# Performance work log

Hardware: AMD Instinct MI355X
Metric: run time of the kernel (lower is better)

## Reference

```python
import jax, jax.numpy as jnp
import numpy as np

DIM = 1024
NUM_HEADS = 16
NUM_KV_HEADS = 4
HEAD_DIM = DIM // NUM_HEADS  # 64
GROUP = NUM_HEADS // NUM_KV_HEADS  # 4
SCALE = HEAD_DIM ** -0.5


def setup_inputs() -> dict:
    key = jax.random.key(0)
    ks = jax.random.split(key, 6)
    B, N = 2, 2048
    x = jax.random.normal(ks[0], (B, N, DIM), dtype=jnp.float32)
    s = DIM ** -0.5
    Wq = jax.random.normal(ks[1], (DIM, DIM), dtype=jnp.float32) * s
    Wk = jax.random.normal(ks[2], (DIM, NUM_KV_HEADS * HEAD_DIM), dtype=jnp.float32) * s
    Wv = jax.random.normal(ks[3], (DIM, NUM_KV_HEADS * HEAD_DIM), dtype=jnp.float32) * s
    Wo = jax.random.normal(ks[4], (DIM, DIM), dtype=jnp.float32) * s
    bo = jax.random.normal(ks[5], (DIM,), dtype=jnp.float32) * 0.01
    return {"x": x, "Wq": Wq, "Wk": Wk, "Wv": Wv, "Wo": Wo, "bo": bo}


def reference(x, Wq, Wk, Wv, Wo, bo):
    B, N, C = x.shape
    # projections
    q = (x @ Wq).reshape(B, N, NUM_HEADS, HEAD_DIM)          # B N H D
    k = (x @ Wk).reshape(B, N, NUM_KV_HEADS, HEAD_DIM)       # B N Kh D
    v = (x @ Wv).reshape(B, N, NUM_KV_HEADS, HEAD_DIM)
    # group query heads: H = Kh * GROUP; broadcast KV per group (no repeat copy)
    q = q.reshape(B, N, NUM_KV_HEADS, GROUP, HEAD_DIM)
    # scores: B Kh G Nq Nk
    attn = jnp.einsum('bqhgd,bkhd->bhgqk', q, k) * SCALE
    attn = jax.nn.softmax(attn, axis=-1)
    out = jnp.einsum('bhgqk,bkhd->bqhgd', attn, v)           # B N Kh G D
    out = out.reshape(B, N, C)
    return out @ Wo + bo
```

## Files before the change

kernel.cpp:

```cpp
#include <hip/hip_runtime.h>


typedef unsigned short u16;
typedef short s8 __attribute__((ext_vector_type(8)));
typedef float f4 __attribute__((ext_vector_type(4)));
typedef u16 u16x4 __attribute__((ext_vector_type(4)));

__device__ __forceinline__ u16 f2bf(float f) {
  unsigned u = __float_as_uint(f);
  u += 0x7fff + ((u >> 16) & 1);
  return (u16)(u >> 16);
}

__device__ __forceinline__ void glds16(const u16* g, u16* l) {
  __builtin_amdgcn_global_load_lds((const __attribute__((address_space(1))) unsigned*)g,
                                   (__attribute__((address_space(3))) unsigned*)l, 16, 0, 0);
}

__global__ __launch_bounds__(256) void cvt_x(const float* __restrict__ x, u16* __restrict__ xb) {
  const int n4 = (4096 * 1024) / 4;
  for (int i = blockIdx.x * 256 + threadIdx.x; i < n4; i += gridDim.x * 256) {
    float4 f = ((const float4*)x)[i];
    u16x4 o = { f2bf(f.x), f2bf(f.y), f2bf(f.z), f2bf(f.w) };
    ((u16x4*)xb)[i] = o;
  }
}

__global__ __launch_bounds__(256) void cvt_w(const float* __restrict__ Wq, const float* __restrict__ Wk,
                                             const float* __restrict__ Wv, const float* __restrict__ Wo,
                                             u16* __restrict__ wqkvt, u16* __restrict__ wot) {
  const int N1 = 1536 * 1024, NT = N1 + 1024 * 1024;
  for (int i = blockIdx.x * 256 + threadIdx.x; i < NT; i += gridDim.x * 256) {
    if (i < N1) {
      int n = i >> 10, k = i & 1023;
      float v;
      if (n < 1024)      v = Wq[(k << 10) + n] * 0.125f;
      else if (n < 1280) v = Wk[(k << 8) + (n - 1024)];
      else               v = Wv[(k << 8) + (n - 1280)];
      wqkvt[i] = f2bf(v);
    } else {
      int j = i - N1;
      int n = j >> 10, k = j & 1023;
      wot[j] = f2bf(Wo[(k << 10) + n]);
    }
  }
}

template<int MODE>
__global__ __launch_bounds__(256) void gemm_bt(const u16* __restrict__ A, const u16* __restrict__ Bt,
                                               u16* __restrict__ Cq, u16* __restrict__ Vt,
                                               float* __restrict__ Cf, const float* __restrict__ bias,
                                               const int K) {
  __shared__ u16 As[128 * 32];
  __shared__ u16 Bs[128 * 32];
  const int tid = threadIdx.x, lane = tid & 63, w = tid >> 6;
  const int wm = w >> 1, wn = w & 1;
  const int m0 = blockIdx.y * 128, n0 = blockIdx.x * 128;
  const int g = lane >> 4, c = lane & 15;
  const int srow = w * 32 + (lane >> 2), scol = (lane & 3) * 8;
  const u16* ga = A + (m0 + srow) * K + scol;
  const u16* gb = Bt + (n0 + srow) * K + scol;
  f4 acc[4][4] = {};
  for (int k0 = 0; k0 < K; k0 += 32) {
    glds16(ga,           &As[w * 1024]);
    glds16(ga + 16 * K,  &As[w * 1024 + 512]);
    glds16(gb,           &Bs[w * 1024]);
    glds16(gb + 16 * K,  &Bs[w * 1024 + 512]);
    ga += 32; gb += 32;
    __syncthreads();
    s8 a[4], b[4];
#pragma unroll
    for (int m = 0; m < 4; ++m) a[m] = *(const s8*)&As[(wm * 64 + m * 16 + c) * 32 + g * 8];
#pragma unroll
    for (int n = 0; n < 4; ++n) b[n] = *(const s8*)&Bs[(wn * 64 + n * 16 + c) * 32 + g * 8];
#pragma unroll
    for (int m = 0; m < 4; ++m)
#pragma unroll
      for (int n = 0; n < 4; ++n)
        acc[m][n] = __builtin_amdgcn_mfma_f32_16x16x32_bf16(a[m], b[n], acc[m][n], 0, 0, 0);
    __syncthreads();
  }
#pragma unroll
  for (int m = 0; m < 4; ++m) {
#pragma unroll
    for (int n = 0; n < 4; ++n) {
#pragma unroll
      for (int r = 0; r < 4; ++r) {
        const int row = m0 + wm * 64 + m * 16 + g * 4 + r;
        const int col = n0 + wn * 64 + n * 16 + c;
        if (MODE == 0) {
          const u16 hv = f2bf(acc[m][n][r]);
          if (col < 1280) {
            Cq[row * 1536 + col] = hv;
          } else {
            const int cc = col - 1280, kh = cc >> 6, dd = cc & 63;
            const int bb = row >> 11, tok = row & 2047;
            Vt[(((bb << 2) + kh) * 64 + dd) * 2048 + tok] = hv;
          }
        } else {
          Cf[row * 1024 + col] = acc[m][n][r] + bias[col];
        }
      }
    }
  }
}

__global__ __launch_bounds__(256) void attn_fwd(const u16* __restrict__ qkv, const u16* __restrict__ vt,
                                                u16* __restrict__ ao) {
  __shared__ u16 QP[64 * 64];
  __shared__ u16 Ks[64 * 64];
  __shared__ u16 Vs[64 * 64];
  const int tid = threadIdx.x, lane = tid & 63, w = tid >> 6;
  const int h = blockIdx.y, b = blockIdx.z, kh = h >> 2;
  const int q0 = blockIdx.x * 64;
  const int g = lane >> 4, c = lane & 15;
  const int srow = w * 16 + (lane >> 3), sch = lane & 7;

#pragma unroll
  for (int j = 0; j < 2; ++j) {
    const int qq = srow + j * 8;
    const int d0 = (sch ^ (qq & 7)) << 3;
    glds16(qkv + (b * 2048 + q0 + qq) * 1536 + h * 64 + d0, &QP[w * 1024 + j * 512]);
  }
  __syncthreads();
  s8 qf[2];
  {
    const int q = w * 16 + c;
#pragma unroll
    for (int ks = 0; ks < 2; ++ks)
      qf[ks] = *(const s8*)&QP[q * 64 + (((ks * 4 + g) ^ (q & 7)) << 3)];
  }
  float mrun = -1e30f, lrun = 0.f;
  f4 acc[4] = {};
  const int kgbase = (b * 2048) * 1536 + 1024 + kh * 64;
  const int vgbase = ((b * 4 + kh) * 64) * 2048;

  for (int kt = 0; kt < 32; ++kt) {
#pragma unroll
    for (int j = 0; j < 2; ++j) {
      const int rr = srow + j * 8;
      const int off = (sch ^ (rr & 7)) << 3;
      glds16(qkv + kgbase + (kt * 64 + rr) * 1536 + off, &Ks[w * 1024 + j * 512]);
      glds16(vt + vgbase + rr * 2048 + kt * 64 + off,    &Vs[w * 1024 + j * 512]);
    }
    __syncthreads();

    f4 s[4];
#pragma unroll
    for (int mf = 0; mf < 4; ++mf) {
      const int key = mf * 16 + c;
      const s8 k0 = *(const s8*)&Ks[key * 64 + ((g ^ (key & 7)) << 3)];
      const s8 k1 = *(const s8*)&Ks[key * 64 + (((4 + g) ^ (key & 7)) << 3)];
      f4 z = {};
      z = __builtin_amdgcn_mfma_f32_16x16x32_bf16(k0, qf[0], z, 0, 0, 0);
      z = __builtin_amdgcn_mfma_f32_16x16x32_bf16(k1, qf[1], z, 0, 0, 0);
      s[mf] = z;
    }
    float tmax = -1e30f;
#pragma unroll
    for (int mf = 0; mf < 4; ++mf)
#pragma unroll
      for (int r = 0; r < 4; ++r) tmax = fmaxf(tmax, s[mf][r]);
    tmax = fmaxf(tmax, __shfl_xor(tmax, 16));
    tmax = fmaxf(tmax, __shfl_xor(tmax, 32));
    const float mnew = fmaxf(mrun, tmax);
    const float fac = __expf(mrun - mnew);
    float p[4][4];
    float psum = 0.f;
#pragma unroll
    for (int mf = 0; mf < 4; ++mf)
#pragma unroll
      for (int r = 0; r < 4; ++r) { p[mf][r] = __expf(s[mf][r] - mnew); psum += p[mf][r]; }
    psum += __shfl_xor(psum, 16);
    psum += __shfl_xor(psum, 32);
    lrun = lrun * fac + psum;
    mrun = mnew;
#pragma unroll
    for (int df = 0; df < 4; ++df)
#pragma unroll
      for (int r = 0; r < 4; ++r) acc[df][r] *= fac;

#pragma unroll
    for (int mf = 0; mf < 4; ++mf) {
      u16x4 ph;
#pragma unroll
      for (int r = 0; r < 4; ++r) ph[r] = f2bf(p[mf][r]);
      const int chp = (mf * 2 + (g >> 1)) ^ (c & 7);
      *(u16x4*)&QP[w * 1024 + c * 64 + chp * 8 + (g & 1) * 4] = ph;
    }
    s8 pb[2];
#pragma unroll
    for (int ks = 0; ks < 2; ++ks)
      pb[ks] = *(const s8*)&QP[w * 1024 + c * 64 + (((ks * 4 + g) ^ (c & 7)) << 3)];

#pragma unroll
    for (int df = 0; df < 4; ++df) {
      const int d = df * 16 + c;
      const s8 v0 = *(const s8*)&Vs[d * 64 + ((g ^ (d & 7)) << 3)];
      const s8 v1 = *(const s8*)&Vs[d * 64 + (((4 + g) ^ (d & 7)) << 3)];
      acc[df] = __builtin_amdgcn_mfma_f32_16x16x32_bf16(v0, pb[0], acc[df], 0, 0, 0);
      acc[df] = __builtin_amdgcn_mfma_f32_16x16x32_bf16(v1, pb[1], acc[df], 0, 0, 0);
    }
    __syncthreads();
  }

  const float inv = 1.f / lrun;
  const int row = b * 2048 + q0 + w * 16 + c;
#pragma unroll
  for (int df = 0; df < 4; ++df) {
    u16x4 o;
#pragma unroll
    for (int r = 0; r < 4; ++r) o[r] = f2bf(acc[df][r] * inv);
    *(u16x4*)&ao[row * 1024 + h * 64 + df * 16 + g * 4] = o;
  }
}

extern "C" void kernel_launch(void* const* d_in, const int* in_sizes, int n_in,
                              void* d_out, int out_size, void* d_ws, size_t ws_size,
                              hipStream_t stream) {
  const float* x  = (const float*)d_in[0];
  const float* Wq = (const float*)d_in[1];
  const float* Wk = (const float*)d_in[2];
  const float* Wv = (const float*)d_in[3];
  const float* Wo = (const float*)d_in[4];
  const float* bo = (const float*)d_in[5];
  float* out = (float*)d_out;

  char* ws = (char*)d_ws;
  u16* xb    = (u16*)(ws);
  u16* ao    = (u16*)(ws);
  u16* wqkvt = (u16*)(ws + 8388608);
  u16* wot   = (u16*)(ws + 11534336);
  u16* qkv   = (u16*)(ws + 13631488);
  u16* vt    = (u16*)(ws + 26214400);

  cvt_x<<<2048, 256, 0, stream>>>(x, xb);
  cvt_w<<<2048, 256, 0, stream>>>(Wq, Wk, Wv, Wo, wqkvt, wot);
  gemm_bt<0><<<dim3(12, 32), 256, 0, stream>>>(xb, wqkvt, qkv, vt, nullptr, nullptr, 1024);
  attn_fwd<<<dim3(32, 16, 2), 256, 0, stream>>>(qkv, vt, ao);
  gemm_bt<1><<<dim3(8, 32), 256, 0, stream>>>(ao, wot, nullptr, nullptr, out, bo, 1024);
}
```

Measured before the change: 225.7 us.

## Double-buffer attention K/V, lazy softmax rescale, tiled weight transpose, compact QKV

Attention now double-buffers the K/V tiles in LDS, so the next tile's global-to-LDS load overlaps compute, and it drops one barrier per iteration. The softmax works in the exp2 domain, with log2e folded into the Q scale, and only rescales the running accumulator when the max grows by more than 8. The weight conversion becomes an LDS-tiled transpose with coalesced reads and writes. QKV is stored with a 1280-wide row, and s_setprio is placed around the MFMA blocks. These changes target memory latency, uncoalesced weight reads and softmax ALU work, at the cost of more LDS use and slightly different numerics from the lazy rescale.

```diff
diff --git a/kernel.cpp b/kernel.cpp
--- a/kernel.cpp
+++ b/kernel.cpp
@@ -1,17 +1,27 @@
 #include <hip/hip_runtime.h>
+#include <hip/hip_bf16.h>
 
 
 typedef unsigned short u16;
 typedef short s8 __attribute__((ext_vector_type(8)));
 typedef float f4 __attribute__((ext_vector_type(4)));
-typedef u16 u16x4 __attribute__((ext_vector_type(4)));
-
-__device__ __forceinline__ u16 f2bf(float f) {
-  unsigned u = __float_as_uint(f);
-  u += 0x7fff + ((u >> 16) & 1);
-  return (u16)(u >> 16);
-}
-
+typedef u16 u16x8 __attribute__((ext_vector_type(8)));
+
+__device__ __forceinline__ unsigned pk2(float a, float b) {
+  __hip_bfloat162 h = __float22bfloat162_rn(make_float2(a, b));
+  unsigned u; __builtin_memcpy(&u, &h, 4); return u;
+}
+__device__ __forceinline__ u16 bf1(float a) {
+  __hip_bfloat16 h = __float2bfloat16(a);
+  u16 u; __builtin_memcpy(&u, &h, 2); return u;
+}
+__device__ __forceinline__ float ex2(float x) {
+#if __has_builtin(__builtin_amdgcn_exp2f)
+  return __builtin_amdgcn_exp2f(x);
+#else
+  return exp2f(x);
+#endif
+}
 __device__ __forceinline__ void glds16(const u16* g, u16* l) {
   __builtin_amdgcn_global_load_lds((const __attribute__((address_space(1))) unsigned*)g,
                                    (__attribute__((address_space(3))) unsigned*)l, 16, 0, 0);
@@ -21,28 +31,41 @@
   const int n4 = (4096 * 1024) / 4;
   for (int i = blockIdx.x * 256 + threadIdx.x; i < n4; i += gridDim.x * 256) {
     float4 f = ((const float4*)x)[i];
-    u16x4 o = { f2bf(f.x), f2bf(f.y), f2bf(f.z), f2bf(f.w) };
-    ((u16x4*)xb)[i] = o;
+    uint2 o; o.x = pk2(f.x, f.y); o.y = pk2(f.z, f.w);
+    ((uint2*)xb)[i] = o;
   }
 }
 
 __global__ __launch_bounds__(256) void cvt_w(const float* __restrict__ Wq, const float* __restrict__ Wk,
                                              const float* __restrict__ Wv, const float* __restrict__ Wo,
                                              u16* __restrict__ wqkvt, u16* __restrict__ wot) {
-  const int N1 = 1536 * 1024, NT = N1 + 1024 * 1024;
-  for (int i = blockIdx.x * 256 + threadIdx.x; i < NT; i += gridDim.x * 256) {
-    if (i < N1) {
-      int n = i >> 10, k = i & 1023;
-      float v;
-      if (n < 1024)      v = Wq[(k << 10) + n] * 0.125f;
-      else if (n < 1280) v = Wk[(k << 8) + (n - 1024)];
-      else               v = Wv[(k << 8) + (n - 1280)];
-      wqkvt[i] = f2bf(v);
-    } else {
-      int j = i - N1;
-      int n = j >> 10, k = j & 1023;
-      wot[j] = f2bf(Wo[(k << 10) + n]);
-    }
+  __shared__ u16 T[64][68];
+  const int m = blockIdx.z;
+  const float* src; u16* dst; int N; int drow0; float scale;
+  if (m == 0)      { src = Wq; N = 1024; dst = wqkvt; drow0 = 0;    scale = 0.18033688011112042f; }
+  else if (m == 1) { src = Wk; N = 256;  dst = wqkvt; drow0 = 1024; scale = 1.f; }
+  else if (m == 2) { src = Wv; N = 256;  dst = wqkvt; drow0 = 1280; scale = 1.f; }
+  else             { src = Wo; N = 1024; dst = wot;   drow0 = 0;    scale = 1.f; }
+  const int n0 = blockIdx.x * 64, k0 = blockIdx.y * 64;
+  if (n0 >= N) return;
+  const int tid = threadIdx.x;
+  const int rr = tid >> 4, cc = (tid & 15) * 4;
+#pragma unroll
+  for (int it = 0; it < 4; ++it) {
+    const int r = rr + it * 16;
+    float4 f = *(const float4*)&src[(k0 + r) * N + n0 + cc];
+    uint2 o; o.x = pk2(f.x * scale, f.y * scale); o.y = pk2(f.z * scale, f.w * scale);
+    *(uint2*)&T[r][cc] = o;
+  }
+  __syncthreads();
+  const int nn = tid >> 3, kq = (tid & 7) * 8;
+#pragma unroll
+  for (int it = 0; it < 2; ++it) {
+    const int n = nn + it * 32;
+    u16x8 v;
+#pragma unroll
+    for (int j = 0; j < 8; ++j) v[j] = T[kq + j][n];
+    *(u16x8*)&dst[(drow0 + n0 + n) * 1024 + k0 + kq] = v;
   }
 }
 
@@ -73,11 +96,13 @@
     for (int m = 0; m < 4; ++m) a[m] = *(const s8*)&As[(wm * 64 + m * 16 + c) * 32 + g * 8];
 #pragma unroll
     for (int n = 0; n < 4; ++n) b[n] = *(const s8*)&Bs[(wn * 64 + n * 16 + c) * 32 + g * 8];
+    __builtin_amdgcn_s_setprio(1);
 #pragma unroll
     for (int m = 0; m < 4; ++m)
 #pragma unroll
       for (int n = 0; n < 4; ++n)
         acc[m][n] = __builtin_amdgcn_mfma_f32_16x16x32_bf16(a[m], b[n], acc[m][n], 0, 0, 0);
+    __builtin_amdgcn_s_setprio(0);
     __syncthreads();
   }
 #pragma unroll
@@ -89,11 +114,11 @@
         const int row = m0 + wm * 64 + m * 16 + g * 4 + r;
         const int col = n0 + wn * 64 + n * 16 + c;
         if (MODE == 0) {
-          const u16 hv = f2bf(acc[m][n][r]);
+          const u16 hv = bf1(acc[m][n][r]);
           if (col < 1280) {
-            Cq[row * 1536 + col] = hv;
+            Cq[row * 1280 + col] = hv;
           } else {
-            const int cc = col - 1280, kh = cc >> 6, dd = cc & 63;
+            const int cc2 = col - 1280, kh = cc2 >> 6, dd = cc2 & 63;
             const int bb = row >> 11, tok = row & 2047;
             Vt[(((bb << 2) + kh) * 64 + dd) * 2048 + tok] = hv;
           }
@@ -108,8 +133,8 @@
 __global__ __launch_bounds__(256) void attn_fwd(const u16* __restrict__ qkv, const u16* __restrict__ vt,
                                                 u16* __restrict__ ao) {
   __shared__ u16 QP[64 * 64];
-  __shared__ u16 Ks[64 * 64];
-  __shared__ u16 Vs[64 * 64];
+  __shared__ u16 Ks[2][64 * 64];
+  __shared__ u16 Vs[2][64 * 64];
   const int tid = threadIdx.x, lane = tid & 63, w = tid >> 6;
   const int h = blockIdx.y, b = blockIdx.z, kh = h >> 2;
   const int q0 = blockIdx.x * 64;
@@ -120,98 +145,104 @@
   for (int j = 0; j < 2; ++j) {
     const int qq = srow + j * 8;
     const int d0 = (sch ^ (qq & 7)) << 3;
-    glds16(qkv + (b * 2048 + q0 + qq) * 1536 + h * 64 + d0, &QP[w * 1024 + j * 512]);
-  }
+    glds16(qkv + (b * 2048 + q0 + qq) * 1280 + h * 64 + d0, &QP[w * 1024 + j * 512]);
+  }
+  const int rr0 = srow, rr1 = srow + 8;
+  const u16* kg0 = qkv + ((b * 2048 + rr0) * 1280) + 1024 + kh * 64 + ((sch ^ (rr0 & 7)) << 3);
+  const u16* kg1 = qkv + ((b * 2048 + rr1) * 1280) + 1024 + kh * 64 + ((sch ^ (rr1 & 7)) << 3);
+  const u16* vg0 = vt + ((b * 4 + kh) * 64 + rr0) * 2048 + ((sch ^ (rr0 & 7)) << 3);
+  const u16* vg1 = vt + ((b * 4 + kh) * 64 + rr1) * 2048 + ((sch ^ (rr1 & 7)) << 3);
+  glds16(kg0, &Ks[0][w * 1024]); glds16(kg1, &Ks[0][w * 1024 + 512]);
+  glds16(vg0, &Vs[0][w * 1024]); glds16(vg1, &Vs[0][w * 1024 + 512]);
   __syncthreads();
+
   s8 qf[2];
   {
     const int q = w * 16 + c;
-#pragma unroll
-    for (int ks = 0; ks < 2; ++ks)
-      qf[ks] = *(const s8*)&QP[q * 64 + (((ks * 4 + g) ^ (q & 7)) << 3)];
-  }
+    qf[0] = *(const s8*)&QP[q * 64 + (((0 + g) ^ (q & 7)) << 3)];
+    qf[1] = *(const s8*)&QP[q * 64 + (((4 + g) ^ (q & 7)) << 3)];
+  }
+  const int kb0 = c * 64 + (((0 + g) ^ (c & 7)) << 3);
+  const int kb1 = c * 64 + (((4 + g) ^ (c & 7)) << 3);
+  const int pwbase = w * 1024 + c * 64;
+
   float mrun = -1e30f, lrun = 0.f;
   f4 acc[4] = {};
-  const int kgbase = (b * 2048) * 1536 + 1024 + kh * 64;
-  const int vgbase = ((b * 4 + kh) * 64) * 2048;
+  int cur = 0;
 
   for (int kt = 0; kt < 32; ++kt) {
-#pragma unroll
-    for (int j = 0; j < 2; ++j) {
-      const int rr = srow + j * 8;
-      const int off = (sch ^ (rr & 7)) << 3;
-      glds16(qkv + kgbase + (kt * 64 + rr) * 1536 + off, &Ks[w * 1024 + j * 512]);
-      glds16(vt + vgbase + rr * 2048 + kt * 64 + off,    &Vs[w * 1024 + j * 512]);
-    }
-    __syncthreads();
-
+    if (kt < 31) {
+      kg0 += 64 * 1280; kg1 += 64 * 1280; vg0 += 64; vg1 += 64;
+      glds16(kg0, &Ks[cur ^ 1][w * 1024]); glds16(kg1, &Ks[cur ^ 1][w * 1024 + 512]);
+      glds16(vg0, &Vs[cur ^ 1][w * 1024]); glds16(vg1, &Vs[cur ^ 1][w * 1024 + 512]);
+    }
     f4 s[4];
+    __builtin_amdgcn_s_setprio(1);
 #pragma unroll
     for (int mf = 0; mf < 4; ++mf) {
-      const int key = mf * 16 + c;
-      const s8 k0 = *(const s8*)&Ks[key * 64 + ((g ^ (key & 7)) << 3)];
-      const s8 k1 = *(const s8*)&Ks[key * 64 + (((4 + g) ^ (key & 7)) << 3)];
+      const s8 k0 = *(const s8*)&Ks[cur][mf * 1024 + kb0];
+      const s8 k1 = *(const s8*)&Ks[cur][mf * 1024 + kb1];
       f4 z = {};
       z = __builtin_amdgcn_mfma_f32_16x16x32_bf16(k0, qf[0], z, 0, 0, 0);
       z = __builtin_amdgcn_mfma_f32_16x16x32_bf16(k1, qf[1], z, 0, 0, 0);
       s[mf] = z;
     }
-    float tmax = -1e30f;
-#pragma unroll
-    for (int mf = 0; mf < 4; ++mf)
+    __builtin_amdgcn_s_setprio(0);
+
+    float tmax = fmaxf(fmaxf(s[0][0], s[0][1]), fmaxf(s[0][2], s[0][3]));
+#pragma unroll
+    for (int mf = 1; mf < 4; ++mf)
 #pragma unroll
       for (int r = 0; r < 4; ++r) tmax = fmaxf(tmax, s[mf][r]);
     tmax = fmaxf(tmax, __shfl_xor(tmax, 16));
     tmax = fmaxf(tmax, __shfl_xor(tmax, 32));
-    const float mnew = fmaxf(mrun, tmax);
-    const float fac = __expf(mrun - mnew);
-    float p[4][4];
-    float psum = 0.f;
+    if (__any(tmax > mrun + 8.f)) {
+      const float mnew = fmaxf(mrun, tmax);
+      const float fac = ex2(mrun - mnew);
+      lrun *= fac;
+#pragma unroll
+      for (int df = 0; df < 4; ++df) acc[df] *= fac;
+      mrun = mnew;
+    }
+    float p[4][4]; float psum = 0.f;
 #pragma unroll
     for (int mf = 0; mf < 4; ++mf)
 #pragma unroll
-      for (int r = 0; r < 4; ++r) { p[mf][r] = __expf(s[mf][r] - mnew); psum += p[mf][r]; }
+      for (int r = 0; r < 4; ++r) { p[mf][r] = ex2(s[mf][r] - mrun); psum += p[mf][r]; }
     psum += __shfl_xor(psum, 16);
     psum += __shfl_xor(psum, 32);
-    lrun = lrun * fac + psum;
-    mrun = mnew;
-#pragma unroll
-    for (int df = 0; df < 4; ++df)
-#pragma unroll
-      for (int r = 0; r < 4; ++r) acc[df][r] *= fac;
+    lrun += psum;
 
 #pragma unroll
     for (int mf = 0; mf < 4; ++mf) {
-      u16x4 ph;
-#pragma unroll
-      for (int r = 0; r < 4; ++r) ph[r] = f2bf(p[mf][r]);
+      uint2 pk; pk.x = pk2(p[mf][0], p[mf][1]); pk.y = pk2(p[mf][2], p[mf][3]);
       const int chp = (mf * 2 + (g >> 1)) ^ (c & 7);
-      *(u16x4*)&QP[w * 1024 + c * 64 + chp * 8 + (g & 1) * 4] = ph;
+      *(uint2*)&QP[pwbase + chp * 8 + (g & 1) * 4] = pk;
     }
     s8 pb[2];
-#pragma unroll
-    for (int ks = 0; ks < 2; ++ks)
-      pb[ks] = *(const s8*)&QP[w * 1024 + c * 64 + (((ks * 4 + g) ^ (c & 7)) << 3)];
-
+    pb[0] = *(const s8*)&QP[pwbase + (((0 + g) ^ (c & 7)) << 3)];
+    pb[1] = *(const s8*)&QP[pwbase + (((4 + g) ^ (c & 7)) << 3)];
+
+    __builtin_amdgcn_s_setprio(1);
 #pragma unroll
     for (int df = 0; df < 4; ++df) {
-      const int d = df * 16 + c;
-      const s8 v0 = *(const s8*)&Vs[d * 64 + ((g ^ (d & 7)) << 3)];
-      const s8 v1 = *(const s8*)&Vs[d * 64 + (((4 + g) ^ (d & 7)) << 3)];
+      const s8 v0 = *(const s8*)&Vs[cur][df * 1024 + kb0];
+      const s8 v1 = *(const s8*)&Vs[cur][df * 1024 + kb1];
       acc[df] = __builtin_amdgcn_mfma_f32_16x16x32_bf16(v0, pb[0], acc[df], 0, 0, 0);
       acc[df] = __builtin_amdgcn_mfma_f32_16x16x32_bf16(v1, pb[1], acc[df], 0, 0, 0);
     }
+    __builtin_amdgcn_s_setprio(0);
     __syncthreads();
+    cur ^= 1;
   }
 
   const float inv = 1.f / lrun;
   const int row = b * 2048 + q0 + w * 16 + c;
 #pragma unroll
   for (int df = 0; df < 4; ++df) {
-    u16x4 o;
-#pragma unroll
-    for (int r = 0; r < 4; ++r) o[r] = f2bf(acc[df][r] * inv);
-    *(u16x4*)&ao[row * 1024 + h * 64 + df * 16 + g * 4] = o;
+    uint2 o; o.x = pk2(acc[df][0] * inv, acc[df][1] * inv);
+    o.y = pk2(acc[df][2] * inv, acc[df][3] * inv);
+    *(uint2*)&ao[row * 1024 + h * 64 + df * 16 + g * 4] = o;
   }
 }
 
@@ -232,11 +263,11 @@
   u16* wqkvt = (u16*)(ws + 8388608);
   u16* wot   = (u16*)(ws + 11534336);
   u16* qkv   = (u16*)(ws + 13631488);
-  u16* vt    = (u16*)(ws + 26214400);
+  u16* vtw   = (u16*)(ws + 24117248);
 
   cvt_x<<<2048, 256, 0, stream>>>(x, xb);
-  cvt_w<<<2048, 256, 0, stream>>>(Wq, Wk, Wv, Wo, wqkvt, wot);
-  gemm_bt<0><<<dim3(12, 32), 256, 0, stream>>>(xb, wqkvt, qkv, vt, nullptr, nullptr, 1024);
-  attn_fwd<<<dim3(32, 16, 2), 256, 0, stream>>>(qkv, vt, ao);
+  cvt_w<<<dim3(16, 16, 4), 256, 0, stream>>>(Wq, Wk, Wv, Wo, wqkvt, wot);
+  gemm_bt<0><<<dim3(12, 32), 256, 0, stream>>>(xb, wqkvt, qkv, vtw, nullptr, nullptr, 1024);
+  attn_fwd<<<dim3(32, 16, 2), 256, 0, stream>>>(qkv, vtw, ao);
   gemm_bt<1><<<dim3(8, 32), 256, 0, stream>>>(ao, wot, nullptr, nullptr, out, bo, 1024);
 }
```

Measured after the change: 211.4 us. -6.4%, faster.
